# Kernel optimization log

Measured on AMD Instinct MI355X. Metric: run time of the kernel, lower is better.

## Reference

```python
import jax, jax.numpy as jnp
import numpy as np

N = 30000      # nodes
E = 480000     # edges (no self loops; GATConv adds them)
IN = 256       # in_features
OUT = 128      # out_features == per-head channels (concat=False)
H = 4          # heads
NEG_SLOPE = 0.2


def setup_inputs() -> dict:
    key = jax.random.key(0)
    k = jax.random.split(key, 6)
    x = jax.random.normal(k[0], (N, IN), dtype=jnp.float32)
    src = jax.random.randint(k[1], (E,), 0, N, dtype=jnp.int32)
    # guarantee no self loops (GATConv would strip them before re-adding)
    off = jax.random.randint(k[2], (E,), 1, N, dtype=jnp.int32)
    dst = (src + off) % N
    edge_index = jnp.stack([src, dst])  # [2, E]
    W = jax.random.normal(k[3], (IN, H * OUT), dtype=jnp.float32) / np.float32(np.sqrt(IN))
    att_src = jax.random.normal(k[4], (H, OUT), dtype=jnp.float32) / np.float32(np.sqrt(OUT))
    att_dst = jax.random.normal(k[5], (H, OUT), dtype=jnp.float32) / np.float32(np.sqrt(OUT))
    bias = jnp.zeros((OUT,), dtype=jnp.float32)
    return {"x": x, "edge_index": edge_index, "W": W,
            "att_src": att_src, "att_dst": att_dst, "bias": bias}


def reference(x, edge_index, W, att_src, att_dst, bias):
    n = x.shape[0]
    # dense projection -> per-head features [N, H, C]
    h = (x @ W).reshape(n, H, OUT)
    a_s = jnp.einsum('nhc,hc->nh', h, att_src)  # [N, H]
    a_d = jnp.einsum('nhc,hc->nh', h, att_dst)  # [N, H]
    # add self loops (GATConv default add_self_loops=True)
    loop = jnp.arange(n, dtype=edge_index.dtype)
    src = jnp.concatenate([edge_index[0], loop])  # [Et]
    dst = jnp.concatenate([edge_index[1], loop])  # [Et]
    # per-edge attention logits + LeakyReLU
    alpha = jax.nn.leaky_relu(a_s[src] + a_d[dst], NEG_SLOPE)  # [Et, H]
    # segment softmax over incoming edges of each dst node
    amax = jax.ops.segment_max(alpha, dst, num_segments=n)      # [N, H]
    ex = jnp.exp(alpha - amax[dst])
    denom = jax.ops.segment_sum(ex, dst, num_segments=n)        # [N, H]
    w = ex / denom[dst]                                          # [Et, H]
    # gather source features, weight, scatter-add to dst
    msg = h[src] * w[:, :, None]                                 # [Et, H, C]
    out = jax.ops.segment_sum(msg, dst, num_segments=n)          # [N, H, C]
    # concat=False -> mean over heads, then bias, then module's tanh
    out = out.mean(axis=1) + bias                                # [N, C]
    return jnp.tanh(out)
```

## Files before the change

### kernel.cpp

```cpp
#include <hip/hip_runtime.h>
#include <math.h>

#define IN_F   256
#define OUT_F  128
#define HEADS  4
#define HD     (HEADS * OUT_F)
#define NEG    0.2f
#define CAP    64

typedef __attribute__((ext_vector_type(8))) short short8;
typedef __attribute__((ext_vector_type(4))) float f32x4;

typedef __attribute__((address_space(1))) const void* gp_t;
typedef __attribute__((address_space(3))) void* lp_t;

static __device__ __forceinline__ ushort f2bf(float f) {
    union { float f; unsigned u; } v; v.f = f;
    unsigned r = (v.u + 0x7FFFu + ((v.u >> 16) & 1u)) >> 16;
    return (ushort)r;
}
static __device__ __forceinline__ float bflo(unsigned u) {
    union { unsigned u; float f; } v; v.u = u << 16; return v.f;
}
static __device__ __forceinline__ float bfhi(unsigned u) {
    union { unsigned u; float f; } v; v.u = u & 0xFFFF0000u; return v.f;
}

__global__ __launch_bounds__(256) void cvt_wt(const float* __restrict__ W,
                                              ushort* __restrict__ WT) {
    int idx = blockIdx.x * blockDim.x + threadIdx.x;
    int n = idx >> 8, k = idx & 255;
    WT[idx] = f2bf(W[k * HD + n]);
}
__global__ __launch_bounds__(256) void calc_va(const float* __restrict__ W,
                                               const float* __restrict__ att_src,
                                               const float* __restrict__ att_dst,
                                               float* __restrict__ va_s,
                                               float* __restrict__ va_d) {
    int idx = blockIdx.x * blockDim.x + threadIdx.x;
    int h = idx >> 8, k = idx & 255;
    const float* wr = W + (size_t)k * HD + h * OUT_F;
    const float* as = att_src + h * OUT_F;
    const float* ad = att_dst + h * OUT_F;
    float ss = 0.f, sd = 0.f;
#pragma unroll 8
    for (int c = 0; c < OUT_F; ++c) {
        float w = wr[c];
        ss = fmaf(w, as[c], ss);
        sd = fmaf(w, ad[c], sd);
    }
    va_s[idx] = ss;
    va_d[idx] = sd;
}

__global__ __launch_bounds__(256) void fused_x(const float* __restrict__ X,
                                               const float* __restrict__ va_s,
                                               const float* __restrict__ va_d,
                                               ushort* __restrict__ Xb,
                                               float* __restrict__ a_s,
                                               float* __restrict__ a_d,
                                               int n_nodes) {
    const int lane = threadIdx.x & 63;
    const int node = blockIdx.x * 4 + (threadIdx.x >> 6);
    if (node >= n_nodes) return;
    float4 v = *(const float4*)(X + (size_t)node * IN_F + lane * 4);
    ushort4 o; o.x = f2bf(v.x); o.y = f2bf(v.y); o.z = f2bf(v.z); o.w = f2bf(v.w);
    *(ushort4*)(Xb + (size_t)node * IN_F + lane * 4) = o;

    float ps[HEADS], pd[HEADS];
#pragma unroll
    for (int hd = 0; hd < HEADS; ++hd) {
        float4 s4 = *(const float4*)(va_s + hd * IN_F + lane * 4);
        float4 d4 = *(const float4*)(va_d + hd * IN_F + lane * 4);
        ps[hd] = v.x * s4.x + v.y * s4.y + v.z * s4.z + v.w * s4.w;
        pd[hd] = v.x * d4.x + v.y * d4.y + v.z * d4.z + v.w * d4.w;
    }
#pragma unroll
    for (int off = 32; off > 0; off >>= 1) {
#pragma unroll
        for (int hd = 0; hd < HEADS; ++hd) {
            ps[hd] += __shfl_xor(ps[hd], off, 64);
            pd[hd] += __shfl_xor(pd[hd], off, 64);
        }
    }
    if (lane == 0) {
        float4 s4 = make_float4(ps[0], ps[1], ps[2], ps[3]);
        float4 d4 = make_float4(pd[0], pd[1], pd[2], pd[3]);
        *(float4*)(a_s + node * 4) = s4;
        *(float4*)(a_d + node * 4) = d4;
    }
}

#define GBM 128
#define GBN 128
#define GBK 32

__global__ __launch_bounds__(256) void gemm_mfma(const ushort* __restrict__ Xb,
                                                 const ushort* __restrict__ WT,
                                                 ushort* __restrict__ Hb,
                                                 int n_nodes) {
    __shared__ ushort As[GBM][GBK];
    __shared__ ushort Bs[GBN][GBK];
    const int tid = threadIdx.x;
    const int m0 = blockIdx.y * GBM;
    const int n0 = blockIdx.x * GBN;
    const int wave = tid >> 6, lane = tid & 63;
    const int wm = (wave & 1) * 64, wn = (wave >> 1) * 64;
    const int l15 = lane & 15, quad = lane >> 4;

    const int rr = lane >> 2;
    const int cg = (lane & 3) ^ ((lane >> 3) & 3);
    const int rA = wave * 16 + rr;
    const ushort* gA0 = Xb + (size_t)(m0 + rA) * IN_F + cg * 8;
    const ushort* gA1 = Xb + (size_t)(m0 + 64 + rA) * IN_F + cg * 8;
    const ushort* gB0 = WT + (size_t)(n0 + rA) * IN_F + cg * 8;
    const ushort* gB1 = WT + (size_t)(n0 + 64 + rA) * IN_F + cg * 8;
    ushort* lA0 = &As[wave * 16][0];
    ushort* lA1 = &As[64 + wave * 16][0];
    ushort* lB0 = &Bs[wave * 16][0];
    ushort* lB1 = &Bs[64 + wave * 16][0];

    f32x4 acc[4][4];
#pragma unroll
    for (int i = 0; i < 4; ++i)
#pragma unroll
        for (int j = 0; j < 4; ++j) acc[i][j] = (f32x4){0.f, 0.f, 0.f, 0.f};

    const int ks = (quad ^ ((l15 >> 1) & 3)) * 8;

    for (int k0 = 0; k0 < IN_F; k0 += GBK) {
        __syncthreads();
        __builtin_amdgcn_global_load_lds((gp_t)(gA0 + k0), (lp_t)lA0, 16, 0, 0);
        __builtin_amdgcn_global_load_lds((gp_t)(gA1 + k0), (lp_t)lA1, 16, 0, 0);
        __builtin_amdgcn_global_load_lds((gp_t)(gB0 + k0), (lp_t)lB0, 16, 0, 0);
        __builtin_amdgcn_global_load_lds((gp_t)(gB1 + k0), (lp_t)lB1, 16, 0, 0);
        __syncthreads();

        short8 af[4], bf_[4];
#pragma unroll
        for (int f = 0; f < 4; ++f) {
            af[f]  = *(const short8*)&As[wm + f * 16 + l15][ks];
            bf_[f] = *(const short8*)&Bs[wn + f * 16 + l15][ks];
        }
#pragma unroll
        for (int fm = 0; fm < 4; ++fm)
#pragma unroll
            for (int fn = 0; fn < 4; ++fn)
                acc[fm][fn] = __builtin_amdgcn_mfma_f32_16x16x32_bf16(
                    af[fm], bf_[fn], acc[fm][fn], 0, 0, 0);
    }

#pragma unroll
    for (int fm = 0; fm < 4; ++fm) {
        int gmb = m0 + wm + fm * 16 + quad * 4;
#pragma unroll
        for (int reg = 0; reg < 4; ++reg) {
            int gm = gmb + reg;
            if (gm < n_nodes) {
#pragma unroll
                for (int fn = 0; fn < 4; ++fn)
                    Hb[(size_t)gm * HD + n0 + wn + fn * 16 + l15] =
                        f2bf(acc[fm][fn][reg]);
            }
        }
    }
}

__global__ __launch_bounds__(256) void build_table(const int* __restrict__ src,
                                                   const int* __restrict__ dst,
                                                   int* __restrict__ cursor,
                                                   int* __restrict__ table,
                                                   int n_edges) {
    int e = blockIdx.x * blockDim.x + threadIdx.x;
    if (e >= n_edges) return;
    int d = dst[e];
    int r = atomicAdd(&cursor[d], 1);
    if (r < CAP) table[(size_t)d * CAP + r] = src[e];
}

__global__ __launch_bounds__(256) void gat_agg(const ushort* __restrict__ Hb,
                                               const float* __restrict__ a_s,
                                               const float* __restrict__ a_d,
                                               const int* __restrict__ cursor,
                                               const int* __restrict__ table,
                                               const float* __restrict__ bias,
                                               float* __restrict__ out,
                                               int n_nodes) {
    const int lane = threadIdx.x & 63;
    const int n = blockIdx.x * 4 + (threadIdx.x >> 6);
    if (n >= n_nodes) return;
    int deg = cursor[n]; if (deg > CAP) deg = CAP;
    const int* row = table + (size_t)n * CAP;
    const unsigned* hbase = (const unsigned*)Hb;

    const float4 ad4 = *(const float4*)(a_d + n * 4);
    const float4 as4 = *(const float4*)(a_s + n * 4);
    const float ad[4] = {ad4.x, ad4.y, ad4.z, ad4.w};
    float aself[4];
    {
        const float asn[4] = {as4.x, as4.y, as4.z, as4.w};
#pragma unroll
        for (int hd = 0; hd < 4; ++hd) {
            float al = asn[hd] + ad[hd];
            aself[hd] = al > 0.f ? al : NEG * al;
        }
    }
    const bool act = lane < deg;
    float al[4];
    {
        int s = act ? row[lane] : 0;
        float4 av = *(const float4*)(a_s + s * 4);
        const float as_[4] = {av.x, av.y, av.z, av.w};
#pragma unroll
        for (int hd = 0; hd < 4; ++hd) {
            float a = as_[hd] + ad[hd];
            a = a > 0.f ? a : NEG * a;
            al[hd] = act ? a : -1e30f;
        }
    }
    float m[4];
#pragma unroll
    for (int hd = 0; hd < 4; ++hd) m[hd] = al[hd];
#pragma unroll
    for (int off = 32; off > 0; off >>= 1)
#pragma unroll
        for (int hd = 0; hd < 4; ++hd)
            m[hd] = fmaxf(m[hd], __shfl_xor(m[hd], off, 64));
#pragma unroll
    for (int hd = 0; hd < 4; ++hd) m[hd] = fmaxf(m[hd], aself[hd]);

    float w[4], den[4], es[4];
#pragma unroll
    for (int hd = 0; hd < 4; ++hd) {
        w[hd] = act ? __expf(al[hd] - m[hd]) : 0.f;
        den[hd] = w[hd];
    }
#pragma unroll
    for (int off = 32; off > 0; off >>= 1)
#pragma unroll
        for (int hd = 0; hd < 4; ++hd)
            den[hd] += __shfl_xor(den[hd], off, 64);
    float rdv[4];
#pragma unroll
    for (int hd = 0; hd < 4; ++hd) {
        es[hd] = __expf(aself[hd] - m[hd]);
        rdv[hd] = 1.f / (den[hd] + es[hd]);
    }

    float acc0[4], acc1[4];
    {
        const unsigned* p = hbase + (size_t)n * 256;
#pragma unroll
        for (int hd = 0; hd < 4; ++hd) {
            unsigned u = p[hd * 64 + lane];
            acc0[hd] = es[hd] * bflo(u);
            acc1[hd] = es[hd] * bfhi(u);
        }
    }
    int e = 0;
    for (; e + 8 <= deg; e += 8) {
        int4 ra = *(const int4*)(row + e);
        int4 rb = *(const int4*)(row + e + 4);
        const unsigned* p[8];
        p[0] = hbase + (size_t)ra.x * 256; p[1] = hbase + (size_t)ra.y * 256;
        p[2] = hbase + (size_t)ra.z * 256; p[3] = hbase + (size_t)ra.w * 256;
        p[4] = hbase + (size_t)rb.x * 256; p[5] = hbase + (size_t)rb.y * 256;
        p[6] = hbase + (size_t)rb.z * 256; p[7] = hbase + (size_t)rb.w * 256;
        unsigned u[8][4];
#pragma unroll
        for (int j = 0; j < 8; ++j)
#pragma unroll
            for (int hd = 0; hd < 4; ++hd)
                u[j][hd] = p[j][hd * 64 + lane];
#pragma unroll
        for (int j = 0; j < 8; ++j) {
#pragma unroll
            for (int hd = 0; hd < 4; ++hd) {
                float wv = __shfl(w[hd], e + j, 64);
                acc0[hd] = fmaf(wv, bflo(u[j][hd]), acc0[hd]);
                acc1[hd] = fmaf(wv, bfhi(u[j][hd]), acc1[hd]);
            }
        }
    }
    for (; e < deg; ++e) {
        int s = row[e];
        const unsigned* p = hbase + (size_t)s * 256;
#pragma unroll
        for (int hd = 0; hd < 4; ++hd) {
            unsigned u = p[hd * 64 + lane];
            float wv = __shfl(w[hd], e, 64);
            acc0[hd] = fmaf(wv, bflo(u), acc0[hd]);
            acc1[hd] = fmaf(wv, bfhi(u), acc1[hd]);
        }
    }
    float o0 = 0.f, o1 = 0.f;
#pragma unroll
    for (int hd = 0; hd < 4; ++hd) {
        o0 = fmaf(acc0[hd], rdv[hd], o0);
        o1 = fmaf(acc1[hd], rdv[hd], o1);
    }
    float2 b = *(const float2*)(bias + 2 * lane);
    o0 = 0.25f * o0 + b.x;
    o1 = 0.25f * o1 + b.y;
    float2 ov = make_float2(tanhf(o0), tanhf(o1));
    *(float2*)(out + (size_t)n * OUT_F + 2 * lane) = ov;
}

extern "C" void kernel_launch(void* const* d_in, const int* in_sizes, int n_in,
                              void* d_out, int out_size, void* d_ws, size_t ws_size,
                              hipStream_t stream) {
    const float* x       = (const float*)d_in[0];
    const int*   ei      = (const int*)d_in[1];
    const float* W       = (const float*)d_in[2];
    const float* att_src = (const float*)d_in[3];
    const float* att_dst = (const float*)d_in[4];
    const float* bias    = (const float*)d_in[5];
    float* out = (float*)d_out;

    const int n_nodes = in_sizes[0] / IN_F;
    const int n_edges = in_sizes[1] / 2;
    const int* src = ei;
    const int* dst = ei + n_edges;

    char* ws = (char*)d_ws;
    size_t off = 0;
    auto alloc = [&](size_t bytes) -> void* {
        void* p = ws + off;
        off = (off + bytes + 255) & ~(size_t)255;
        return p;
    };
    ushort* Xb     = (ushort*)alloc((size_t)n_nodes * IN_F * sizeof(ushort));
    ushort* Hb     = (ushort*)alloc((size_t)n_nodes * HD * sizeof(ushort));
    ushort* WT     = (ushort*)alloc((size_t)HD * IN_F * sizeof(ushort));
    float*  va_s   = (float*)alloc((size_t)HEADS * IN_F * sizeof(float));
    float*  va_d   = (float*)alloc((size_t)HEADS * IN_F * sizeof(float));
    float*  a_s    = (float*)alloc((size_t)n_nodes * HEADS * sizeof(float));
    float*  a_d    = (float*)alloc((size_t)n_nodes * HEADS * sizeof(float));
    int*    cursor = (int*)alloc((size_t)n_nodes * sizeof(int));
    int*    table  = (int*)alloc((size_t)n_nodes * CAP * sizeof(int));
    (void)ws_size; (void)n_in; (void)out_size;

    hipMemsetAsync(cursor, 0, (size_t)n_nodes * sizeof(int), stream);

    cvt_wt<<<(HD * IN_F) / 256, 256, 0, stream>>>(W, WT);
    calc_va<<<(HEADS * IN_F) / 256, 256, 0, stream>>>(W, att_src, att_dst, va_s, va_d);
    fused_x<<<(n_nodes + 3) / 4, 256, 0, stream>>>(x, va_s, va_d, Xb, a_s, a_d, n_nodes);
    build_table<<<(n_edges + 255) / 256, 256, 0, stream>>>(src, dst, cursor, table, n_edges);

    dim3 ggrid(HD / GBN, (n_nodes + GBM - 1) / GBM);
    gemm_mfma<<<ggrid, 256, 0, stream>>>(Xb, WT, Hb, n_nodes);

    gat_agg<<<(n_nodes + 3) / 4, 256, 0, stream>>>(Hb, a_s, a_d, cursor, table,
                                                   bias, out, n_nodes);
}
```

Before: 229.9 us.

## Interleave head features per lane and stage softmax weights in LDS

Adds a transpose kernel that repacks the bf16 H matrix so each lane's four head values sit in one 16-byte uint4, letting the aggregation gather one vector load per neighbor instead of four scalar loads. Softmax weights move from per-edge shuffles into shared memory and are read as float4 broadcasts. This costs an extra kernel pass that reads and writes the whole H (about 30 MB each way), plus a block-wide barrier.

```diff
diff --git a/kernel.cpp b/kernel.cpp
--- a/kernel.cpp
+++ b/kernel.cpp
@@ -166,6 +166,20 @@
     }
 }
 
+__global__ __launch_bounds__(256) void transpose_h(const unsigned* __restrict__ Hbu,
+                                                   uint4* __restrict__ Hc, int n_nodes) {
+    const int lane = threadIdx.x & 63;
+    const int n = blockIdx.x * 4 + (threadIdx.x >> 6);
+    if (n >= n_nodes) return;
+    const unsigned* p = Hbu + (size_t)n * 256;
+    uint4 v;
+    v.x = p[lane];
+    v.y = p[64 + lane];
+    v.z = p[128 + lane];
+    v.w = p[192 + lane];
+    Hc[(size_t)n * 64 + lane] = v;
+}
+
 __global__ __launch_bounds__(256) void build_table(const int* __restrict__ src,
                                                    const int* __restrict__ dst,
                                                    int* __restrict__ cursor,
@@ -178,7 +192,7 @@
     if (r < CAP) table[(size_t)d * CAP + r] = src[e];
 }
 
-__global__ __launch_bounds__(256) void gat_agg(const ushort* __restrict__ Hb,
+__global__ __launch_bounds__(256) void gat_agg(const uint4* __restrict__ Hc,
                                                const float* __restrict__ a_s,
                                                const float* __restrict__ a_d,
                                                const int* __restrict__ cursor,
@@ -186,112 +200,122 @@
                                                const float* __restrict__ bias,
                                                float* __restrict__ out,
                                                int n_nodes) {
+    __shared__ float wsh[4][CAP][4];
+    const int wv = threadIdx.x >> 6;
     const int lane = threadIdx.x & 63;
-    const int n = blockIdx.x * 4 + (threadIdx.x >> 6);
-    if (n >= n_nodes) return;
-    int deg = cursor[n]; if (deg > CAP) deg = CAP;
-    const int* row = table + (size_t)n * CAP;
-    const unsigned* hbase = (const unsigned*)Hb;
-
-    const float4 ad4 = *(const float4*)(a_d + n * 4);
-    const float4 as4 = *(const float4*)(a_s + n * 4);
-    const float ad[4] = {ad4.x, ad4.y, ad4.z, ad4.w};
-    float aself[4];
-    {
-        const float asn[4] = {as4.x, as4.y, as4.z, as4.w};
+    const int n = blockIdx.x * 4 + wv;
+    const bool valid = n < n_nodes;
+
+    int deg = 0;
+    const int* row = table;
+    float es[4], rdv[4];
+    if (valid) {
+        deg = cursor[n]; if (deg > CAP) deg = CAP;
+        row = table + (size_t)n * CAP;
+
+        const float4 ad4 = *(const float4*)(a_d + n * 4);
+        const float4 as4 = *(const float4*)(a_s + n * 4);
+        const float ad[4] = {ad4.x, ad4.y, ad4.z, ad4.w};
+        float aself[4];
+        {
+            const float asn[4] = {as4.x, as4.y, as4.z, as4.w};
+#pragma unroll
+            for (int hd = 0; hd < 4; ++hd) {
+                float al = asn[hd] + ad[hd];
+                aself[hd] = al > 0.f ? al : NEG * al;
+            }
+        }
+        const bool act = lane < deg;
+        float al[4];
+        {
+            int s = act ? row[lane] : 0;
+            float4 av = *(const float4*)(a_s + s * 4);
+            const float as_[4] = {av.x, av.y, av.z, av.w};
+#pragma unroll
+            for (int hd = 0; hd < 4; ++hd) {
+                float a = as_[hd] + ad[hd];
+                a = a > 0.f ? a : NEG * a;
+                al[hd] = act ? a : -1e30f;
+            }
+        }
+        float m[4];
+#pragma unroll
+        for (int hd = 0; hd < 4; ++hd) m[hd] = al[hd];
+#pragma unroll
+        for (int off = 32; off > 0; off >>= 1)
+#pragma unroll
+            for (int hd = 0; hd < 4; ++hd)
+                m[hd] = fmaxf(m[hd], __shfl_xor(m[hd], off, 64));
+#pragma unroll
+        for (int hd = 0; hd < 4; ++hd) m[hd] = fmaxf(m[hd], aself[hd]);
+
+        float w[4], den[4];
 #pragma unroll
         for (int hd = 0; hd < 4; ++hd) {
-            float al = asn[hd] + ad[hd];
-            aself[hd] = al > 0.f ? al : NEG * al;
-        }
-    }
-    const bool act = lane < deg;
-    float al[4];
-    {
-        int s = act ? row[lane] : 0;
-        float4 av = *(const float4*)(a_s + s * 4);
-        const float as_[4] = {av.x, av.y, av.z, av.w};
+            w[hd] = act ? __expf(al[hd] - m[hd]) : 0.f;
+            den[hd] = w[hd];
+        }
+#pragma unroll
+        for (int off = 32; off > 0; off >>= 1)
+#pragma unroll
+            for (int hd = 0; hd < 4; ++hd)
+                den[hd] += __shfl_xor(den[hd], off, 64);
 #pragma unroll
         for (int hd = 0; hd < 4; ++hd) {
-            float a = as_[hd] + ad[hd];
-            a = a > 0.f ? a : NEG * a;
-            al[hd] = act ? a : -1e30f;
-        }
-    }
-    float m[4];
-#pragma unroll
-    for (int hd = 0; hd < 4; ++hd) m[hd] = al[hd];
-#pragma unroll
-    for (int off = 32; off > 0; off >>= 1)
-#pragma unroll
-        for (int hd = 0; hd < 4; ++hd)
-            m[hd] = fmaxf(m[hd], __shfl_xor(m[hd], off, 64));
-#pragma unroll
-    for (int hd = 0; hd < 4; ++hd) m[hd] = fmaxf(m[hd], aself[hd]);
-
-    float w[4], den[4], es[4];
-#pragma unroll
-    for (int hd = 0; hd < 4; ++hd) {
-        w[hd] = act ? __expf(al[hd] - m[hd]) : 0.f;
-        den[hd] = w[hd];
-    }
-#pragma unroll
-    for (int off = 32; off > 0; off >>= 1)
-#pragma unroll
-        for (int hd = 0; hd < 4; ++hd)
-            den[hd] += __shfl_xor(den[hd], off, 64);
-    float rdv[4];
-#pragma unroll
-    for (int hd = 0; hd < 4; ++hd) {
-        es[hd] = __expf(aself[hd] - m[hd]);
-        rdv[hd] = 1.f / (den[hd] + es[hd]);
-    }
+            es[hd] = __expf(aself[hd] - m[hd]);
+            rdv[hd] = 1.f / (den[hd] + es[hd]);
+        }
+        *(float4*)&wsh[wv][lane][0] = make_float4(w[0], w[1], w[2], w[3]);
+    }
+    __syncthreads();
+    if (!valid) return;
 
     float acc0[4], acc1[4];
     {
-        const unsigned* p = hbase + (size_t)n * 256;
-#pragma unroll
-        for (int hd = 0; hd < 4; ++hd) {
-            unsigned u = p[hd * 64 + lane];
-            acc0[hd] = es[hd] * bflo(u);
-            acc1[hd] = es[hd] * bfhi(u);
-        }
+        uint4 u = Hc[(size_t)n * 64 + lane];
+        acc0[0] = es[0] * bflo(u.x); acc1[0] = es[0] * bfhi(u.x);
+        acc0[1] = es[1] * bflo(u.y); acc1[1] = es[1] * bfhi(u.y);
+        acc0[2] = es[2] * bflo(u.z); acc1[2] = es[2] * bfhi(u.z);
+        acc0[3] = es[3] * bflo(u.w); acc1[3] = es[3] * bfhi(u.w);
     }
     int e = 0;
     for (; e + 8 <= deg; e += 8) {
         int4 ra = *(const int4*)(row + e);
         int4 rb = *(const int4*)(row + e + 4);
-        const unsigned* p[8];
-        p[0] = hbase + (size_t)ra.x * 256; p[1] = hbase + (size_t)ra.y * 256;
-        p[2] = hbase + (size_t)ra.z * 256; p[3] = hbase + (size_t)ra.w * 256;
-        p[4] = hbase + (size_t)rb.x * 256; p[5] = hbase + (size_t)rb.y * 256;
-        p[6] = hbase + (size_t)rb.z * 256; p[7] = hbase + (size_t)rb.w * 256;
-        unsigned u[8][4];
-#pragma unroll
-        for (int j = 0; j < 8; ++j)
-#pragma unroll
-            for (int hd = 0; hd < 4; ++hd)
-                u[j][hd] = p[j][hd * 64 + lane];
+        uint4 u[8];
+        u[0] = Hc[(size_t)ra.x * 64 + lane];
+        u[1] = Hc[(size_t)ra.y * 64 + lane];
+        u[2] = Hc[(size_t)ra.z * 64 + lane];
+        u[3] = Hc[(size_t)ra.w * 64 + lane];
+        u[4] = Hc[(size_t)rb.x * 64 + lane];
+        u[5] = Hc[(size_t)rb.y * 64 + lane];
+        u[6] = Hc[(size_t)rb.z * 64 + lane];
+        u[7] = Hc[(size_t)rb.w * 64 + lane];
 #pragma unroll
         for (int j = 0; j < 8; ++j) {
-#pragma unroll
-            for (int hd = 0; hd < 4; ++hd) {
-                float wv = __shfl(w[hd], e + j, 64);
-                acc0[hd] = fmaf(wv, bflo(u[j][hd]), acc0[hd]);
-                acc1[hd] = fmaf(wv, bfhi(u[j][hd]), acc1[hd]);
-            }
+            float4 w4 = *(const float4*)&wsh[wv][e + j][0];
+            acc0[0] = fmaf(w4.x, bflo(u[j].x), acc0[0]);
+            acc1[0] = fmaf(w4.x, bfhi(u[j].x), acc1[0]);
+            acc0[1] = fmaf(w4.y, bflo(u[j].y), acc0[1]);
+            acc1[1] = fmaf(w4.y, bfhi(u[j].y), acc1[1]);
+            acc0[2] = fmaf(w4.z, bflo(u[j].z), acc0[2]);
+            acc1[2] = fmaf(w4.z, bfhi(u[j].z), acc1[2]);
+            acc0[3] = fmaf(w4.w, bflo(u[j].w), acc0[3]);
+            acc1[3] = fmaf(w4.w, bfhi(u[j].w), acc1[3]);
         }
     }
     for (; e < deg; ++e) {
         int s = row[e];
-        const unsigned* p = hbase + (size_t)s * 256;
-#pragma unroll
-        for (int hd = 0; hd < 4; ++hd) {
-            unsigned u = p[hd * 64 + lane];
-            float wv = __shfl(w[hd], e, 64);
-            acc0[hd] = fmaf(wv, bflo(u), acc0[hd]);
-            acc1[hd] = fmaf(wv, bfhi(u), acc1[hd]);
-        }
+        uint4 u = Hc[(size_t)s * 64 + lane];
+        float4 w4 = *(const float4*)&wsh[wv][e][0];
+        acc0[0] = fmaf(w4.x, bflo(u.x), acc0[0]);
+        acc1[0] = fmaf(w4.x, bfhi(u.x), acc1[0]);
+        acc0[1] = fmaf(w4.y, bflo(u.y), acc0[1]);
+        acc1[1] = fmaf(w4.y, bfhi(u.y), acc1[1]);
+        acc0[2] = fmaf(w4.z, bflo(u.z), acc0[2]);
+        acc1[2] = fmaf(w4.z, bfhi(u.z), acc1[2]);
+        acc0[3] = fmaf(w4.w, bflo(u.w), acc0[3]);
+        acc1[3] = fmaf(w4.w, bfhi(u.w), acc1[3]);
     }
     float o0 = 0.f, o1 = 0.f;
 #pragma unroll
@@ -331,6 +355,7 @@
     };
     ushort* Xb     = (ushort*)alloc((size_t)n_nodes * IN_F * sizeof(ushort));
     ushort* Hb     = (ushort*)alloc((size_t)n_nodes * HD * sizeof(ushort));
+    uint4*  Hc     = (uint4*)alloc((size_t)n_nodes * 64 * sizeof(uint4));
     ushort* WT     = (ushort*)alloc((size_t)HD * IN_F * sizeof(ushort));
     float*  va_s   = (float*)alloc((size_t)HEADS * IN_F * sizeof(float));
     float*  va_d   = (float*)alloc((size_t)HEADS * IN_F * sizeof(float));
@@ -349,7 +374,8 @@
 
     dim3 ggrid(HD / GBN, (n_nodes + GBM - 1) / GBM);
     gemm_mfma<<<ggrid, 256, 0, stream>>>(Xb, WT, Hb, n_nodes);
-
-    gat_agg<<<(n_nodes + 3) / 4, 256, 0, stream>>>(Hb, a_s, a_d, cursor, table,
+    transpose_h<<<(n_nodes + 3) / 4, 256, 0, stream>>>((const unsigned*)Hb, Hc, n_nodes);
+
+    gat_agg<<<(n_nodes + 3) / 4, 256, 0, stream>>>(Hc, a_s, a_d, cursor, table,
                                                    bias, out, n_nodes);
 }
```

Measured after the change: 235.6 us. 1.02x slower.
